# Optimization experiments

Measured on AMD Instinct MI355X. Metric: run time of the kernel, lower is better.

## Reference

```python
import jax, jax.numpy as jnp
import numpy as np

INPUT_SIZE, HIDDEN_SIZE, OUTPUT_SIZE = 2, 512, 512
ALPHA = 0.1


def setup_inputs() -> dict:
    key = jax.random.key(0)
    ks = jax.random.split(key, 8)
    B, T = 256, 512
    inputs = jax.random.normal(ks[0], (B, T, INPUT_SIZE), dtype=jnp.float32)
    init_context = jax.random.normal(ks[1], (B, OUTPUT_SIZE), dtype=jnp.float32)
    # parameters (torch Linear convention: y = x @ W.T + b)
    W_in = jax.random.normal(ks[2], (HIDDEN_SIZE, INPUT_SIZE), dtype=jnp.float32) * (1.0 / np.sqrt(INPUT_SIZE + HIDDEN_SIZE))
    b_in = jnp.zeros((HIDDEN_SIZE,), dtype=jnp.float32)
    # orthogonal-ish recurrent weight via QR
    A = jax.random.normal(ks[3], (HIDDEN_SIZE, HIDDEN_SIZE), dtype=jnp.float32)
    W_rec, _ = jnp.linalg.qr(A)
    W_rec = W_rec.astype(jnp.float32)
    b_rec = jnp.zeros((HIDDEN_SIZE,), dtype=jnp.float32)
    W_out = jax.random.normal(ks[4], (OUTPUT_SIZE, HIDDEN_SIZE), dtype=jnp.float32) * (1.0 / np.sqrt(HIDDEN_SIZE + OUTPUT_SIZE))
    W_h_init = jax.random.normal(ks[5], (HIDDEN_SIZE, OUTPUT_SIZE), dtype=jnp.float32) * (1.0 / np.sqrt(HIDDEN_SIZE + OUTPUT_SIZE))
    return {"inputs": inputs, "init_context": init_context, "W_in": W_in, "b_in": b_in,
            "W_rec": W_rec, "b_rec": b_rec, "W_out": W_out, "W_h_init": W_h_init}


def reference(inputs, init_context, W_in, b_in, W_rec, b_rec, W_out, W_h_init):
    # inputs: (B, T, I); init_context: (B, O)
    h0 = init_context @ W_h_init.T  # (B, H)
    # precompute input projection for all timesteps: (B, T, H)
    x_proj = jnp.einsum('bti,hi->bth', inputs, W_in) + b_in

    def step(h, x_t):
        h_new = (1.0 - ALPHA) * h + ALPHA * jnp.tanh(x_t + h @ W_rec.T + b_rec)
        return h_new, h_new

    # scan over time: move T to leading axis
    _, hs = jax.lax.scan(step, h0, jnp.swapaxes(x_proj, 0, 1))  # hs: (T, B, H)
    hidden_states = jnp.swapaxes(hs, 0, 1)  # (B, T, H)
    outputs = jnp.einsum('bth,oh->bto', hidden_states, W_out)  # (B, T, O)
    return hidden_states, outputs
```

## Files before the change

### kernel.cpp

```cpp
#include <hip/hip_runtime.h>

typedef __bf16 bf16x8 __attribute__((ext_vector_type(8)));
typedef float f32x4 __attribute__((ext_vector_type(4)));

union UQ { uint4 q; bf16x8 v; };

__device__ __forceinline__ unsigned short f2bf(float x){
  union { float f; unsigned u; } c; c.f = x;
  return (unsigned short)((c.u + 0x7fffu + ((c.u >> 16) & 1u)) >> 16);
}

__global__ void zero_flags(int* __restrict__ p){
  p[blockIdx.x * 256 + threadIdx.x] = 0;
}

__global__ void pack_kernel(const float* __restrict__ W, uint4* __restrict__ dst){
  int tid  = blockIdx.x * 512 + threadIdx.x;
  int lane = tid & 63;
  int kt   = (tid >> 6) & 15;
  int ntl  = tid >> 10;
  int row  = ntl * 16 + (lane & 15);
  int k0   = kt * 32 + ((lane >> 4) << 3);
  const float* s = &W[row * 512 + k0];
  unsigned a0 = f2bf(s[0]) | ((unsigned)f2bf(s[1]) << 16);
  unsigned a1 = f2bf(s[2]) | ((unsigned)f2bf(s[3]) << 16);
  unsigned a2 = f2bf(s[4]) | ((unsigned)f2bf(s[5]) << 16);
  unsigned a3 = f2bf(s[6]) | ((unsigned)f2bf(s[7]) << 16);
  dst[tid] = (uint4){a0, a1, a2, a3};
}

__global__ void h0_kernel(const float* __restrict__ init, const float* __restrict__ Whi,
                          float* __restrict__ h0, unsigned short* __restrict__ hb0){
  int b = blockIdx.x, n = threadIdx.x;
  __shared__ float ic[512];
  ic[n] = init[b * 512 + n];
  __syncthreads();
  const float4* wr = (const float4*)&Whi[n * 512];
  float s = 0.f;
  #pragma unroll 8
  for (int o = 0; o < 128; o++){
    float4 w = wr[o];
    s += w.x * ic[4*o] + w.y * ic[4*o+1] + w.z * ic[4*o+2] + w.w * ic[4*o+3];
  }
  h0[b * 512 + n] = s;
  hb0[b * 512 + n] = f2bf(s);
}

__global__ __launch_bounds__(512, 2)
void rnn_kernel(const float* __restrict__ inputs, const float* __restrict__ W_in,
                const float* __restrict__ b_in, const float* __restrict__ b_rec,
                const uint4* __restrict__ wfrag, const float* __restrict__ h0,
                const unsigned short* __restrict__ hb0,
                unsigned short* __restrict__ xbuf, int* __restrict__ flags,
                float* __restrict__ hidden){
  const int m    = blockIdx.x & 15, sl = blockIdx.x >> 4;
  const int g16  = m << 4;
  const int tid  = threadIdx.x, w = tid >> 6, lane = tid & 63;
  const int col  = lane & 15, quad = lane >> 4;
  const int nbase = (sl << 8) + (w << 5);

  __shared__ unsigned short hbuf[2][16 * 512];
  __shared__ float xin_s[2][32];

  UQ u0[16], u1[16];
  {
    const int nt0 = nbase >> 4;
    #pragma unroll
    for (int kt = 0; kt < 16; kt++){
      u0[kt].q = wfrag[((nt0 * 16) + kt) * 64 + lane];
      u1[kt].q = wfrag[(((nt0 + 1) * 16) + kt) * 64 + lane];
    }
  }

  float win0[8], win1[8], bcv[8];
  #pragma unroll
  for (int i = 0; i < 2; i++)
    #pragma unroll
    for (int r = 0; r < 4; r++){
      int n = nbase + i * 16 + (quad << 2) + r;
      win0[i*4+r] = W_in[2*n];  win1[i*4+r] = W_in[2*n+1];
      bcv[i*4+r]  = b_in[n] + b_rec[n];
    }

  float h[8];
  #pragma unroll
  for (int i = 0; i < 2; i++){
    float4 h4 = *(const float4*)&h0[(g16 + col) * 512 + nbase + i * 16 + (quad << 2)];
    h[i*4+0] = h4.x; h[i*4+1] = h4.y; h[i*4+2] = h4.z; h[i*4+3] = h4.w;
  }

  {
    int b = tid >> 5, n0 = (tid & 31) << 4;
    const uint4* s4 = (const uint4*)&hb0[(g16 + b) * 512 + n0];
    uint4 v0 = s4[0], v1 = s4[1];
    int sw = (b & 7) << 3;
    *(uint4*)&hbuf[0][b * 512 + (n0 ^ sw)]       = v0;
    *(uint4*)&hbuf[0][b * 512 + ((n0 + 8) ^ sw)] = v1;
  }
  if (tid < 32) xin_s[0][tid] = inputs[((g16 + (tid >> 1)) * 512 + 0) * 2 + (tid & 1)];

  int* flg_my = flags + ((sl * 16 + m) << 9);
  int* flg_pr = flags + (((1 - sl) * 16 + m) << 9);
  unsigned long long* xm = (unsigned long long*)(xbuf + (m << 14));
  const int prow = tid >> 5;
  const int pn0  = ((1 - sl) << 8) + ((tid & 31) << 3);
  unsigned long long own[2] = {0ull, 0ull};

  for (int t = 0; t < 512; t++){
    const int s = t & 1;
    if (t > 0){
      const int swc = (col & 7) << 3;
      #pragma unroll
      for (int i = 0; i < 2; i++){
        int n = nbase + i * 16 + (quad << 2);
        *(unsigned long long*)&hbuf[s][col * 512 + (n ^ swc)] = own[i];
      }
      while (__hip_atomic_load(&flg_pr[t - 1], __ATOMIC_RELAXED, __HIP_MEMORY_SCOPE_AGENT) == 0) {}
      unsigned long long p0 = __hip_atomic_load(&xm[(s << 11) + (prow << 7) + (pn0 >> 2)],
                                                __ATOMIC_RELAXED, __HIP_MEMORY_SCOPE_AGENT);
      unsigned long long p1 = __hip_atomic_load(&xm[(s << 11) + (prow << 7) + (pn0 >> 2) + 1],
                                                __ATOMIC_RELAXED, __HIP_MEMORY_SCOPE_AGENT);
      const int swb = (prow & 7) << 3;
      union { unsigned long long d; uint2 u; } c0, c1;
      c0.d = p0; c1.d = p1;
      *(uint4*)&hbuf[s][prow * 512 + (pn0 ^ swb)] = (uint4){c0.u.x, c0.u.y, c1.u.x, c1.u.y};
    }
    __syncthreads();

    if (t < 511 && tid < 32)
      xin_s[(t + 1) & 1][tid] = inputs[((g16 + (tid >> 1)) * 512 + (t + 1)) * 2 + (tid & 1)];

    f32x4 acc0 = {0.f,0.f,0.f,0.f}, acc1 = {0.f,0.f,0.f,0.f};
    #pragma unroll
    for (int kt = 0; kt < 16; kt++){
      UQ a;
      a.q = *(const uint4*)&hbuf[s][col * 512 + (((kt << 5) + (quad << 3)) ^ ((col & 7) << 3))];
      acc0 = __builtin_amdgcn_mfma_f32_16x16x32_bf16(u0[kt].v, a.v, acc0, 0, 0, 0);
      acc1 = __builtin_amdgcn_mfma_f32_16x16x32_bf16(u1[kt].v, a.v, acc1, 0, 0, 0);
    }

    const float x0 = xin_s[s][2 * col], x1 = xin_s[s][2 * col + 1];
    unsigned short us[8];
    #pragma unroll
    for (int i = 0; i < 2; i++)
      #pragma unroll
      for (int r = 0; r < 4; r++){
        float zz = (i ? acc1[r] : acc0[r])
                 + fmaf(x0, win0[i*4+r], fmaf(x1, win1[i*4+r], bcv[i*4+r]));
        float e  = __expf(2.0f * zz);
        float th = 1.0f - 2.0f / (e + 1.0f);
        h[i*4+r] = 0.9f * h[i*4+r] + 0.1f * th;
        us[i*4+r] = f2bf(h[i*4+r]);
      }
    own[0] = (unsigned long long)us[0] | ((unsigned long long)us[1] << 16)
           | ((unsigned long long)us[2] << 32) | ((unsigned long long)us[3] << 48);
    own[1] = (unsigned long long)us[4] | ((unsigned long long)us[5] << 16)
           | ((unsigned long long)us[6] << 32) | ((unsigned long long)us[7] << 48);

    if (t < 511){
      const int ns = (t + 1) & 1;
      #pragma unroll
      for (int i = 0; i < 2; i++){
        int n = nbase + i * 16 + (quad << 2);
        unsigned long long old = __hip_atomic_exchange(
            &xm[(ns << 11) + (col << 7) + (n >> 2)], own[i],
            __ATOMIC_RELAXED, __HIP_MEMORY_SCOPE_AGENT);
        asm volatile("" :: "v"(old));
      }
      asm volatile("s_waitcnt vmcnt(0)" ::: "memory");
      __syncthreads();
      if (tid == 0)
        __hip_atomic_store(&flg_my[t], 1, __ATOMIC_RELAXED, __HIP_MEMORY_SCOPE_AGENT);
    }

    #pragma unroll
    for (int i = 0; i < 2; i++)
      *(float4*)&hidden[((size_t)(g16 + col) * 512 + t) * 512 + nbase + i * 16 + (quad << 2)] =
          (float4){h[i*4+0], h[i*4+1], h[i*4+2], h[i*4+3]};
  }
}

__global__ __launch_bounds__(512, 2)
void out_gemm(const float* __restrict__ hidden, const uint4* __restrict__ wofrag,
              float* __restrict__ outp){
  const int tid  = threadIdx.x;
  const int w    = tid >> 6;
  const int lane = tid & 63;
  const int col  = lane & 15;
  const int quad = lane >> 4;
  const int ms   = w >> 1;
  const int nh   = w & 1;
  const int m0   = blockIdx.x << 7;

  __shared__ unsigned short albf[128 * 32];

  f32x4 acc[2][16];
  #pragma unroll
  for (int mt = 0; mt < 2; mt++)
    #pragma unroll
    for (int nt = 0; nt < 16; nt++) acc[mt][nt] = (f32x4){0.f, 0.f, 0.f, 0.f};

  for (int kt = 0; kt < 16; kt++){
    #pragma unroll
    for (int i = 0; i < 2; i++){
      int r  = (tid >> 3) + (i << 6);
      int c4 = (tid & 7) << 2;
      float4 v = *(const float4*)&hidden[(m0 + r) * 512 + (kt << 5) + c4];
      unsigned lo = f2bf(v.x) | ((unsigned)f2bf(v.y) << 16);
      unsigned hi = f2bf(v.z) | ((unsigned)f2bf(v.w) << 16);
      int byteoff = (r << 6) + ((c4 << 1) ^ (((r >> 1) & 3) << 4));
      *(uint2*)((char*)albf + byteoff) = (uint2){lo, hi};
    }
    __syncthreads();

    bf16x8 af[2];
    #pragma unroll
    for (int mt = 0; mt < 2; mt++){
      int rl = (ms << 5) + (mt << 4) + col;
      int byteoff = (rl << 6) + ((quad << 4) ^ (((rl >> 1) & 3) << 4));
      af[mt] = *(const bf16x8*)((const char*)albf + byteoff);
    }

    #pragma unroll
    for (int nt = 0; nt < 16; nt++){
      UQ u; u.q = wofrag[((((nh << 4) + nt) << 4) + kt) * 64 + lane];
      acc[0][nt] = __builtin_amdgcn_mfma_f32_16x16x32_bf16(af[0], u.v, acc[0][nt], 0, 0, 0);
      acc[1][nt] = __builtin_amdgcn_mfma_f32_16x16x32_bf16(af[1], u.v, acc[1][nt], 0, 0, 0);
    }
    __syncthreads();
  }

  #pragma unroll
  for (int mt = 0; mt < 2; mt++)
    #pragma unroll
    for (int nt = 0; nt < 16; nt++)
      #pragma unroll
      for (int r = 0; r < 4; r++)
        outp[(m0 + (ms << 5) + (mt << 4) + (quad << 2) + r) * 512
             + (nh << 8) + (nt << 4) + col] = acc[mt][nt][r];
}

extern "C" void kernel_launch(void* const* d_in, const int* in_sizes, int n_in,
                              void* d_out, int out_size, void* d_ws, size_t ws_size,
                              hipStream_t stream){
  const float* inputs  = (const float*)d_in[0];
  const float* initc   = (const float*)d_in[1];
  const float* W_in    = (const float*)d_in[2];
  const float* b_in    = (const float*)d_in[3];
  const float* W_rec   = (const float*)d_in[4];
  const float* b_rec   = (const float*)d_in[5];
  const float* W_out   = (const float*)d_in[6];
  const float* W_hi    = (const float*)d_in[7];

  float* hidden  = (float*)d_out;
  float* outputs = hidden + (size_t)67108864;

  char* ws = (char*)d_ws;
  uint4*          wrec_f = (uint4*)ws;
  uint4*          wout_f = (uint4*)(ws + (512 << 10));
  float*          h0     = (float*)(ws + (1024 << 10));
  unsigned short* hb0    = (unsigned short*)(ws + (1536 << 10));
  unsigned short* xbuf   = (unsigned short*)(ws + (1792 << 10));
  int*            flags  = (int*)(ws + (2304 << 10));

  zero_flags<<<64, 256, 0, stream>>>(flags);
  pack_kernel<<<64, 512, 0, stream>>>(W_rec, wrec_f);
  pack_kernel<<<64, 512, 0, stream>>>(W_out, wout_f);
  h0_kernel<<<256, 512, 0, stream>>>(initc, W_hi, h0, hb0);
  rnn_kernel<<<32, 512, 0, stream>>>(inputs, W_in, b_in, b_rec, wrec_f, h0, hb0,
                                     xbuf, flags, hidden);
  out_gemm<<<1024, 512, 0, stream>>>(hidden, wout_f, outputs);
}
```

Measured before the change: 1.822 ms.

## Split RNN step into local-LDS and remote-register halves with per-wave flags

Each block now keeps only its own half of the hidden state in LDS and loads the peer block's half straight from global memory into registers for the MFMA, so the K loop splits into a local part and a remote part. The block-wide barrier before the cross-block flag store is replaced by per-wave atomic increments, and consumers spin on a count of 8 from a single lane. This cuts barriers and LDS staging on the serial recurrence critical path. The costs are more register pressure, per-wave atomics, and reliance on relaxed-ordering visibility between waves.

Result: slower. 3.024 ms (+66.0%).

```diff
diff --git a/kernel.cpp b/kernel.cpp
--- a/kernel.cpp
+++ b/kernel.cpp
@@ -2,8 +2,9 @@
 
 typedef __bf16 bf16x8 __attribute__((ext_vector_type(8)));
 typedef float f32x4 __attribute__((ext_vector_type(4)));
-
-union UQ { uint4 q; bf16x8 v; };
+typedef unsigned int u32x4 __attribute__((ext_vector_type(4)));
+
+union UQ { uint4 q; u32x4 p; bf16x8 v; unsigned long long d[2]; };
 
 __device__ __forceinline__ unsigned short f2bf(float x){
   union { float f; unsigned u; } c; c.f = x;
@@ -53,22 +54,31 @@
                 const unsigned short* __restrict__ hb0,
                 unsigned short* __restrict__ xbuf, int* __restrict__ flags,
                 float* __restrict__ hidden){
-  const int m    = blockIdx.x & 15, sl = blockIdx.x >> 4;
-  const int g16  = m << 4;
-  const int tid  = threadIdx.x, w = tid >> 6, lane = tid & 63;
-  const int col  = lane & 15, quad = lane >> 4;
+  const int bid = blockIdx.x;
+  const int m = bid & 15, sl = bid >> 4;
+  const int g16 = m << 4;
+  const int tid = threadIdx.x, w = tid >> 6, lane = tid & 63;
+  const int col = lane & 15, quad = lane >> 4;
   const int nbase = (sl << 8) + (w << 5);
-
-  __shared__ unsigned short hbuf[2][16 * 512];
+  const int own8  = sl << 3;
+  const int pbase = (1 - sl) << 8;
+
+  __shared__ unsigned short hbuf[2][16 * 256];
   __shared__ float xin_s[2][32];
 
   UQ u0[16], u1[16];
   {
     const int nt0 = nbase >> 4;
     #pragma unroll
-    for (int kt = 0; kt < 16; kt++){
-      u0[kt].q = wfrag[((nt0 * 16) + kt) * 64 + lane];
-      u1[kt].q = wfrag[(((nt0 + 1) * 16) + kt) * 64 + lane];
+    for (int j = 0; j < 16; j++){
+      int kt = (own8 + j) & 15;
+      u0[j].q = wfrag[(nt0 * 16 + kt) * 64 + lane];
+      u1[j].q = wfrag[((nt0 + 1) * 16 + kt) * 64 + lane];
+    }
+    #pragma unroll
+    for (int j = 0; j < 16; j++){
+      asm volatile("" : "+v"(u0[j].d[0]), "+v"(u0[j].d[1]));
+      asm volatile("" : "+v"(u1[j].d[0]), "+v"(u1[j].d[1]));
     }
   }
 
@@ -90,56 +100,57 @@
   }
 
   {
-    int b = tid >> 5, n0 = (tid & 31) << 4;
-    const uint4* s4 = (const uint4*)&hb0[(g16 + b) * 512 + n0];
-    uint4 v0 = s4[0], v1 = s4[1];
-    int sw = (b & 7) << 3;
-    *(uint4*)&hbuf[0][b * 512 + (n0 ^ sw)]       = v0;
-    *(uint4*)&hbuf[0][b * 512 + ((n0 + 8) ^ sw)] = v1;
+    int b = tid >> 5, n0 = (tid & 31) << 3;
+    uint4 v = *(const uint4*)&hb0[(g16 + b) * 512 + (sl << 8) + n0];
+    *(uint4*)&hbuf[0][(b << 8) + (n0 ^ ((b & 7) << 3))] = v;
   }
   if (tid < 32) xin_s[0][tid] = inputs[((g16 + (tid >> 1)) * 512 + 0) * 2 + (tid & 1)];
+  __syncthreads();
 
   int* flg_my = flags + ((sl * 16 + m) << 9);
   int* flg_pr = flags + (((1 - sl) * 16 + m) << 9);
-  unsigned long long* xm = (unsigned long long*)(xbuf + (m << 14));
-  const int prow = tid >> 5;
-  const int pn0  = ((1 - sl) << 8) + ((tid & 31) << 3);
-  unsigned long long own[2] = {0ull, 0ull};
+  unsigned long long* xm = (unsigned long long*)xbuf + ((size_t)m << 12);
+  const int swc = (col & 7) << 3;
 
   for (int t = 0; t < 512; t++){
-    const int s = t & 1;
-    if (t > 0){
-      const int swc = (col & 7) << 3;
-      #pragma unroll
-      for (int i = 0; i < 2; i++){
-        int n = nbase + i * 16 + (quad << 2);
-        *(unsigned long long*)&hbuf[s][col * 512 + (n ^ swc)] = own[i];
+    const int ls = t & 1;
+    const int ps = ls ^ 1;
+
+    UQ pa[8];
+    if (t == 0){
+      #pragma unroll
+      for (int kk = 0; kk < 8; kk++)
+        pa[kk].q = *(const uint4*)&hb0[(g16 + col) * 512 + pbase + (kk << 5) + (quad << 3)];
+    } else {
+      if (lane == 0)
+        while (__hip_atomic_load(&flg_pr[t - 1], __ATOMIC_RELAXED,
+                                 __HIP_MEMORY_SCOPE_AGENT) < 8) {}
+      const unsigned long long* psrc =
+          xm + ((size_t)ps << 11) + (col << 7) + (pbase >> 2) + (quad << 1);
+      #pragma unroll
+      for (int kk = 0; kk < 8; kk++){
+        pa[kk].d[0] = __hip_atomic_load(psrc + (kk << 3),
+                        __ATOMIC_RELAXED, __HIP_MEMORY_SCOPE_AGENT);
+        pa[kk].d[1] = __hip_atomic_load(psrc + (kk << 3) + 1,
+                        __ATOMIC_RELAXED, __HIP_MEMORY_SCOPE_AGENT);
       }
-      while (__hip_atomic_load(&flg_pr[t - 1], __ATOMIC_RELAXED, __HIP_MEMORY_SCOPE_AGENT) == 0) {}
-      unsigned long long p0 = __hip_atomic_load(&xm[(s << 11) + (prow << 7) + (pn0 >> 2)],
-                                                __ATOMIC_RELAXED, __HIP_MEMORY_SCOPE_AGENT);
-      unsigned long long p1 = __hip_atomic_load(&xm[(s << 11) + (prow << 7) + (pn0 >> 2) + 1],
-                                                __ATOMIC_RELAXED, __HIP_MEMORY_SCOPE_AGENT);
-      const int swb = (prow & 7) << 3;
-      union { unsigned long long d; uint2 u; } c0, c1;
-      c0.d = p0; c1.d = p1;
-      *(uint4*)&hbuf[s][prow * 512 + (pn0 ^ swb)] = (uint4){c0.u.x, c0.u.y, c1.u.x, c1.u.y};
-    }
-    __syncthreads();
-
-    if (t < 511 && tid < 32)
-      xin_s[(t + 1) & 1][tid] = inputs[((g16 + (tid >> 1)) * 512 + (t + 1)) * 2 + (tid & 1)];
+    }
 
     f32x4 acc0 = {0.f,0.f,0.f,0.f}, acc1 = {0.f,0.f,0.f,0.f};
     #pragma unroll
-    for (int kt = 0; kt < 16; kt++){
+    for (int kk = 0; kk < 8; kk++){
       UQ a;
-      a.q = *(const uint4*)&hbuf[s][col * 512 + (((kt << 5) + (quad << 3)) ^ ((col & 7) << 3))];
-      acc0 = __builtin_amdgcn_mfma_f32_16x16x32_bf16(u0[kt].v, a.v, acc0, 0, 0, 0);
-      acc1 = __builtin_amdgcn_mfma_f32_16x16x32_bf16(u1[kt].v, a.v, acc1, 0, 0, 0);
-    }
-
-    const float x0 = xin_s[s][2 * col], x1 = xin_s[s][2 * col + 1];
+      a.q = *(const uint4*)&hbuf[ls][(col << 8) + ((((kk << 5) + (quad << 3))) ^ swc)];
+      acc0 = __builtin_amdgcn_mfma_f32_16x16x32_bf16(u0[kk].v, a.v, acc0, 0, 0, 0);
+      acc1 = __builtin_amdgcn_mfma_f32_16x16x32_bf16(u1[kk].v, a.v, acc1, 0, 0, 0);
+    }
+    #pragma unroll
+    for (int kk = 0; kk < 8; kk++){
+      acc0 = __builtin_amdgcn_mfma_f32_16x16x32_bf16(u0[8+kk].v, pa[kk].v, acc0, 0, 0, 0);
+      acc1 = __builtin_amdgcn_mfma_f32_16x16x32_bf16(u1[8+kk].v, pa[kk].v, acc1, 0, 0, 0);
+    }
+
+    const float x0 = xin_s[ls][2 * col], x1 = xin_s[ls][2 * col + 1];
     unsigned short us[8];
     #pragma unroll
     for (int i = 0; i < 2; i++)
@@ -152,31 +163,42 @@
         h[i*4+r] = 0.9f * h[i*4+r] + 0.1f * th;
         us[i*4+r] = f2bf(h[i*4+r]);
       }
-    own[0] = (unsigned long long)us[0] | ((unsigned long long)us[1] << 16)
-           | ((unsigned long long)us[2] << 32) | ((unsigned long long)us[3] << 48);
-    own[1] = (unsigned long long)us[4] | ((unsigned long long)us[5] << 16)
-           | ((unsigned long long)us[6] << 32) | ((unsigned long long)us[7] << 48);
+    unsigned long long own0 =
+        (unsigned long long)us[0] | ((unsigned long long)us[1] << 16)
+      | ((unsigned long long)us[2] << 32) | ((unsigned long long)us[3] << 48);
+    unsigned long long own1 =
+        (unsigned long long)us[4] | ((unsigned long long)us[5] << 16)
+      | ((unsigned long long)us[6] << 32) | ((unsigned long long)us[7] << 48);
 
     if (t < 511){
-      const int ns = (t + 1) & 1;
-      #pragma unroll
-      for (int i = 0; i < 2; i++){
-        int n = nbase + i * 16 + (quad << 2);
-        unsigned long long old = __hip_atomic_exchange(
-            &xm[(ns << 11) + (col << 7) + (n >> 2)], own[i],
-            __ATOMIC_RELAXED, __HIP_MEMORY_SCOPE_AGENT);
-        asm volatile("" :: "v"(old));
-      }
+      unsigned long long* xdst = xm + ((size_t)ls << 11) + (col << 7) + (nbase >> 2) + quad;
+      unsigned long long o0 = __hip_atomic_exchange(xdst, own0,
+                                __ATOMIC_RELAXED, __HIP_MEMORY_SCOPE_AGENT);
+      unsigned long long o1 = __hip_atomic_exchange(xdst + 4, own1,
+                                __ATOMIC_RELAXED, __HIP_MEMORY_SCOPE_AGENT);
+      asm volatile("" :: "v"(o0), "v"(o1));
+    }
+
+    #pragma unroll
+    for (int i = 0; i < 2; i++){
+      int nloc = (w << 5) + (i << 4) + (quad << 2);
+      *(unsigned long long*)&hbuf[ls ^ 1][(col << 8) + (nloc ^ swc)] = (i ? own1 : own0);
+    }
+    if (tid < 32 && t < 511)
+      xin_s[ls ^ 1][tid] = inputs[((g16 + (tid >> 1)) * 512 + (t + 1)) * 2 + (tid & 1)];
+
+    if (t < 511){
       asm volatile("s_waitcnt vmcnt(0)" ::: "memory");
-      __syncthreads();
-      if (tid == 0)
-        __hip_atomic_store(&flg_my[t], 1, __ATOMIC_RELAXED, __HIP_MEMORY_SCOPE_AGENT);
+      if (lane == 0)
+        __hip_atomic_fetch_add(&flg_my[t], 1, __ATOMIC_RELAXED, __HIP_MEMORY_SCOPE_AGENT);
     }
 
     #pragma unroll
     for (int i = 0; i < 2; i++)
       *(float4*)&hidden[((size_t)(g16 + col) * 512 + t) * 512 + nbase + i * 16 + (quad << 2)] =
           (float4){h[i*4+0], h[i*4+1], h[i*4+2], h[i*4+3]};
+
+    __syncthreads();
   }
 }
 
```
